# Kernel optimization log

Measured on AMD Instinct MI355X. Metric: run time of the kernel, lower is better.

## Reference

```python
import jax, jax.numpy as jnp
import numpy as np

EMBED_DIM = 1024
NUM_HEADS = 16
HEAD_DIM = EMBED_DIM // NUM_HEADS


def setup_inputs() -> dict:
    key = jax.random.key(0)
    ks = jax.random.split(key, 5)
    B, S, D = 2, 2048, EMBED_DIM
    scale = 1.0 / np.sqrt(D)
    x = jax.random.normal(ks[0], (B, S, D), dtype=jnp.float32)
    qkv_w = jax.random.uniform(ks[1], (3 * D, D), dtype=jnp.float32, minval=-scale, maxval=scale)
    qkv_b = jax.random.uniform(ks[2], (3 * D,), dtype=jnp.float32, minval=-scale, maxval=scale)
    out_w = jax.random.uniform(ks[3], (D, D), dtype=jnp.float32, minval=-scale, maxval=scale)
    out_b = jax.random.uniform(ks[4], (D,), dtype=jnp.float32, minval=-scale, maxval=scale)
    return {"x": x, "qkv_w": qkv_w, "qkv_b": qkv_b, "out_w": out_w, "out_b": out_b}


def reference(x, qkv_w, qkv_b, out_w, out_b):
    B, S, D = x.shape
    H, hd = NUM_HEADS, HEAD_DIM
    # QKV projection (torch Linear: y = x @ W^T + b)
    qkv = jnp.einsum('bsd,ed->bse', x, qkv_w) + qkv_b          # [B,S,3D]
    qkv = qkv.reshape(B, S, 3, H, hd)
    q, k, v = (jnp.moveaxis(qkv[:, :, i], 2, 1) for i in range(3))  # each [B,H,S,hd]
    scores = jnp.einsum('bhqd,bhkd->bhqk', q, k) / np.sqrt(hd)  # [B,H,S,S]
    probs = jax.nn.softmax(scores, axis=-1)
    attn = jnp.einsum('bhqk,bhkd->bhqd', probs, v)              # [B,H,S,hd]
    attn = jnp.moveaxis(attn, 1, 2).reshape(B, S, D)
    return jnp.einsum('bsd,ed->bse', attn, out_w) + out_b
```

## Files before the change

kernel.cpp:

```cpp
#include <hip/hip_runtime.h>
#include <stdint.h>

typedef __bf16 bf16;
typedef __attribute__((ext_vector_type(2))) __bf16 bf16x2;
typedef __attribute__((ext_vector_type(4))) __bf16 bf16x4;
typedef __attribute__((ext_vector_type(8))) __bf16 bf16x8;
typedef __attribute__((ext_vector_type(4))) float f32x4;
typedef __attribute__((ext_vector_type(16))) float f32x16;

#define LOG2E_OVER_8 0.18033688011112042f

#if __has_builtin(__builtin_amdgcn_exp2f)
#define EXP2(x) __builtin_amdgcn_exp2f(x)
#else
#define EXP2(x) exp2f(x)
#endif

__device__ __forceinline__ void gl_lds16(const bf16* g, bf16* l) {
  __builtin_amdgcn_global_load_lds(
      (const __attribute__((address_space(1))) void*)g,
      (__attribute__((address_space(3))) void*)l, 16, 0, 0);
}
#define WAIT_VM0_BARRIER() asm volatile("s_waitcnt vmcnt(0)\n\ts_barrier" ::: "memory")

__device__ __forceinline__ uint32_t pack2(float a, float b) {
  union { bf16x2 v; uint32_t u; } z;
  z.v[0] = (bf16)a; z.v[1] = (bf16)b;
  return z.u;
}

__global__ __launch_bounds__(256) void cvt_kernel(const float* __restrict__ s,
                                                  bf16* __restrict__ d, int n) {
  int i = (blockIdx.x * 256 + threadIdx.x) * 8;
  if (i >= n) return;
  float4 a = *(const float4*)(s + i);
  float4 b = *(const float4*)(s + i + 4);
  bf16x8 o;
  o[0] = (bf16)a.x; o[1] = (bf16)a.y; o[2] = (bf16)a.z; o[3] = (bf16)a.w;
  o[4] = (bf16)b.x; o[5] = (bf16)b.y; o[6] = (bf16)b.z; o[7] = (bf16)b.w;
  *(bf16x8*)(d + i) = o;
}

template <int EPI>
__global__ __launch_bounds__(256, 3) void gemm_bt(
    const bf16* __restrict__ A, const bf16* __restrict__ Bw,
    const float* __restrict__ bias,
    bf16* __restrict__ qo, bf16* __restrict__ ko, bf16* __restrict__ vTo,
    float* __restrict__ outF) {
  constexpr int MT = EPI ? 64 : 128;
  constexpr int MI = MT / 32;
  constexpr int ASZ = MT * 32;
  constexpr int BSZ = 128 * 32;
  constexpr int RS = 136;
  constexpr int SME = EPI ? (2 * ASZ + 2 * BSZ) : (128 * RS);
  __shared__ __attribute__((aligned(16))) bf16 smem[SME];

  int bx, by;
  {
    const int f = blockIdx.x;
    const int xcd = f & 7, idx = f >> 3;
    if constexpr (EPI == 0) { by = xcd * 4 + (idx & 3); bx = idx >> 2; }
    else                    { by = xcd * 8 + (idx & 7); bx = idx >> 3; }
  }

  const int t = threadIdx.x;
  const int L = t & 63;
  const int li = L & 15;
  const int qd = L >> 4;
  const int w = t >> 6;
  const int wm = (w >> 1) * (MT / 2);
  const int wn = (w & 1) * 64;
  const int bm0 = by * MT;
  const int bn0 = bx * 128;
  const int r_st = t >> 2;
  const int c_st = (t & 3) * 8;

  const bf16* Ab = A + (size_t)bm0 * 1024;
  const bf16* Bb = Bw + (size_t)bn0 * 1024;

  auto issue = [&](int k0, int bi) {
    bf16* As_ = smem + bi * ASZ;
    bf16* Bs_ = smem + 2 * ASZ + bi * BSZ;
    gl_lds16(Ab + (size_t)r_st * 1024 + k0 + c_st, As_ + t * 8);
    if constexpr (MT == 128)
      gl_lds16(Ab + (size_t)(r_st + 64) * 1024 + k0 + c_st, As_ + (t + 256) * 8);
    gl_lds16(Bb + (size_t)r_st * 1024 + k0 + c_st, Bs_ + t * 8);
    gl_lds16(Bb + (size_t)(r_st + 64) * 1024 + k0 + c_st, Bs_ + (t + 256) * 8);
  };

  f32x4 acc[MI][4] = {};
  issue(0, 0);
  for (int it = 0; it < 32; ++it) {
    WAIT_VM0_BARRIER();
    if (it < 31) issue((it + 1) * 32, (it + 1) & 1);
    const bf16* Ac = smem + (it & 1) * ASZ;
    const bf16* Bc = smem + 2 * ASZ + (it & 1) * BSZ;
    bf16x8 af[MI], bfr[4];
#pragma unroll
    for (int mi = 0; mi < MI; ++mi)
      af[mi] = *(const bf16x8*)(Ac + (wm + mi * 16 + li) * 32 + qd * 8);
#pragma unroll
    for (int ni = 0; ni < 4; ++ni)
      bfr[ni] = *(const bf16x8*)(Bc + (wn + ni * 16 + li) * 32 + qd * 8);
#pragma unroll
    for (int mi = 0; mi < MI; ++mi)
#pragma unroll
      for (int ni = 0; ni < 4; ++ni)
        acc[mi][ni] = __builtin_amdgcn_mfma_f32_16x16x32_bf16(af[mi], bfr[ni],
                                                              acc[mi][ni], 0, 0, 0);
  }

  if constexpr (EPI == 0) {
    const int which = bn0 >> 10;
    __syncthreads();
    bf16* Ct = smem;
    if (which == 2) {
#pragma unroll
      for (int mi = 0; mi < MI; ++mi) {
        const int m_l = wm + mi * 16 + qd * 4;
#pragma unroll
        for (int ni = 0; ni < 4; ++ni) {
          const int n_l = wn + ni * 16 + li;
          const float bi = bias[bn0 + n_l];
          bf16x4 pk;
#pragma unroll
          for (int r = 0; r < 4; ++r) pk[r] = (bf16)(acc[mi][ni][r] + bi);
          *(bf16x4*)(Ct + n_l * RS + m_l) = pk;
        }
      }
    } else {
      const float sc = (which == 0) ? LOG2E_OVER_8 : 1.0f;
#pragma unroll
      for (int mi = 0; mi < MI; ++mi) {
        const int m_l = wm + mi * 16 + qd * 4;
#pragma unroll
        for (int ni = 0; ni < 4; ++ni) {
          const int n_l = wn + ni * 16 + li;
          const float bi = bias[bn0 + n_l];
#pragma unroll
          for (int r = 0; r < 4; ++r)
            Ct[(m_l + r) * RS + n_l] = (bf16)((acc[mi][ni][r] + bi) * sc);
        }
      }
    }
    __syncthreads();
    const int jr = t >> 4;
    const int jc = t & 15;
#pragma unroll
    for (int pass = 0; pass < 8; ++pass) {
      const int row = pass * 16 + jr;
      bf16x8 vv = *(const bf16x8*)(Ct + row * RS + jc * 8);
      if (which == 2) {
        const int n_g = bn0 + row;
        const int hh = (n_g >> 6) & 15, dd = n_g & 63;
        const int bb = bm0 >> 11;
        const int s_b = (bm0 & 2047) + jc * 8;
        *(bf16x8*)(vTo + ((size_t)(bb * 16 + hh) * 64 + dd) * 2048 + s_b) = vv;
      } else {
        const int m_g = bm0 + row;
        const int bb = m_g >> 11, ss = m_g & 2047;
        const int n_g = bn0 + jc * 8;
        const int hh = (n_g >> 6) & 15, dd = n_g & 63;
        bf16* dst = (which == 0 ? qo : ko);
        *(bf16x8*)(dst + ((size_t)(bb * 16 + hh) * 2048 + ss) * 64 + dd) = vv;
      }
    }
  } else {
#pragma unroll
    for (int mi = 0; mi < MI; ++mi) {
      const int m_g = bm0 + wm + mi * 16 + qd * 4;
#pragma unroll
      for (int ni = 0; ni < 4; ++ni) {
        const int n_g = bn0 + wn + ni * 16 + li;
        const float bi = bias[n_g];
#pragma unroll
        for (int r = 0; r < 4; ++r)
          outF[(size_t)(m_g + r) * 1024 + n_g] = acc[mi][ni][r] + bi;
      }
    }
  }
}

__global__ __launch_bounds__(128, 2) void attn_fwd(
    const bf16* __restrict__ Q, const bf16* __restrict__ K,
    const bf16* __restrict__ VT, bf16* __restrict__ AO) {
  __shared__ __attribute__((aligned(16))) bf16 Ks[2 * 4096];
  __shared__ __attribute__((aligned(16))) bf16 Vs[2 * 4096];
  const int t = threadIdx.x;
  const int L = t & 63;
  const int m31 = L & 31;
  const int hi = L >> 5;
  const int w = t >> 6;

  const int lid = blockIdx.x;
  const int bh_ = ((lid & 7) << 2) + (lid >> 8);
  const int qb = (lid >> 3) & 31;
  const int b = bh_ >> 4, h = bh_ & 15;
  const size_t bh = (size_t)(b * 16 + h);

  const bf16* Qp = Q + bh * 2048 * 64;
  const bf16* Kp = K + bh * 2048 * 64;
  const bf16* Vp = VT + bh * 64 * 2048;
  const int q0 = qb * 64 + w * 32;

  bf16x8 qf[4];
#pragma unroll
  for (int s = 0; s < 4; ++s)
    qf[s] = *(const bf16x8*)(Qp + (size_t)(q0 + m31) * 64 + s * 16 + hi * 8);

  f32x16 acc[2] = {};
  float lsum = 0.f;

  const int srow = t >> 3;
  const int scc = (t & 7) ^ (srow & 7);
  auto issue = [&](int kt, int bi) {
    const bf16* Kt = Kp + (size_t)kt * 4096;
    const bf16* Vt = Vp + kt * 64;
    bf16* Kd = Ks + bi * 4096;
    bf16* Vd = Vs + bi * 4096;
#pragma unroll
    for (int r = 0; r < 4; ++r) {
      gl_lds16(Kt + (srow + 16 * r) * 64 + scc * 8, Kd + (t + 128 * r) * 8);
      gl_lds16(Vt + (size_t)(srow + 16 * r) * 2048 + scc * 8, Vd + (t + 128 * r) * 8);
    }
  };

  const int rlow = m31 & 7;
  issue(0, 0);
  for (int kt = 0; kt < 32; ++kt) {
    WAIT_VM0_BARRIER();
    if (kt < 31) issue(kt + 1, (kt + 1) & 1);
    const bf16* Kc = Ks + (kt & 1) * 4096;
    const bf16* Vc = Vs + (kt & 1) * 4096;

    f32x16 st[2];
#pragma unroll
    for (int kt2 = 0; kt2 < 2; ++kt2) {
      f32x16 z = {};
#pragma unroll
      for (int s = 0; s < 4; ++s) {
        bf16x8 kf = *(const bf16x8*)(
            Kc + ((kt2 * 32 + m31) * 8 + ((2 * s + hi) ^ rlow)) * 8);
        z = __builtin_amdgcn_mfma_f32_32x32x16_bf16(kf, qf[s], z, 0, 0, 0);
      }
      st[kt2] = z;
    }

    uint32_t pk[2][8];
#pragma unroll
    for (int kt2 = 0; kt2 < 2; ++kt2)
#pragma unroll
      for (int j = 0; j < 8; ++j) {
        float a = EXP2(st[kt2][2 * j]);
        float c = EXP2(st[kt2][2 * j + 1]);
        lsum += a + c;
        pk[kt2][j] = pack2(a, c);
      }

    uint32_t sw[2][8];
#pragma unroll
    for (int kt2 = 0; kt2 < 2; ++kt2)
#pragma unroll
      for (int j = 0; j < 8; ++j)
        sw[kt2][j] = (uint32_t)__shfl_xor((int)pk[kt2][j], 32);

    union FU { uint32_t u[4]; bf16x8 v; };
    FU af[2][2];
#pragma unroll
    for (int kt2 = 0; kt2 < 2; ++kt2) {
      if (hi == 0) {
        af[kt2][0].u[0] = pk[kt2][0]; af[kt2][0].u[1] = pk[kt2][1];
        af[kt2][0].u[2] = sw[kt2][0]; af[kt2][0].u[3] = sw[kt2][1];
        af[kt2][1].u[0] = pk[kt2][4]; af[kt2][1].u[1] = pk[kt2][5];
        af[kt2][1].u[2] = sw[kt2][4]; af[kt2][1].u[3] = sw[kt2][5];
      } else {
        af[kt2][0].u[0] = sw[kt2][2]; af[kt2][0].u[1] = sw[kt2][3];
        af[kt2][0].u[2] = pk[kt2][2]; af[kt2][0].u[3] = pk[kt2][3];
        af[kt2][1].u[0] = sw[kt2][6]; af[kt2][1].u[1] = sw[kt2][7];
        af[kt2][1].u[2] = pk[kt2][6]; af[kt2][1].u[3] = pk[kt2][7];
      }
    }

#pragma unroll
    for (int dt = 0; dt < 2; ++dt)
#pragma unroll
      for (int kt2 = 0; kt2 < 2; ++kt2)
#pragma unroll
        for (int u = 0; u < 2; ++u) {
          bf16x8 vf = *(const bf16x8*)(
              Vc + ((dt * 32 + m31) * 8 + ((kt2 * 4 + u * 2 + hi) ^ rlow)) * 8);
          acc[dt] = __builtin_amdgcn_mfma_f32_32x32x16_bf16(af[kt2][u].v, vf,
                                                            acc[dt], 0, 0, 0);
        }
  }

  lsum += __shfl_xor(lsum, 32);
  const float inv = 1.f / lsum;

#pragma unroll
  for (int r = 0; r < 16; ++r) {
    const int qrow = (r & 3) + 8 * (r >> 2) + 4 * hi;
    const float invq = __shfl(inv, qrow);
    const size_t base = ((size_t)b * 2048 + q0 + qrow) * 1024 + h * 64 + m31;
    AO[base] = (bf16)(acc[0][r] * invq);
    AO[base + 32] = (bf16)(acc[1][r] * invq);
  }
}

extern "C" void kernel_launch(void* const* d_in, const int* in_sizes, int n_in,
                              void* d_out, int out_size, void* d_ws, size_t ws_size,
                              hipStream_t stream) {
  const float* x = (const float*)d_in[0];
  const float* qkvw = (const float*)d_in[1];
  const float* qkvb = (const float*)d_in[2];
  const float* outw = (const float*)d_in[3];
  const float* outb = (const float*)d_in[4];
  float* out = (float*)d_out;

  bf16* xb = (bf16*)d_ws;
  bf16* wq = xb + (size_t)4096 * 1024;
  bf16* wo = wq + (size_t)3072 * 1024;
  bf16* q = wo + (size_t)1024 * 1024;
  bf16* kk = q + (size_t)2 * 16 * 2048 * 64;
  bf16* vT = kk + (size_t)2 * 16 * 2048 * 64;
  bf16* attn = xb;

  cvt_kernel<<<2048, 256, 0, stream>>>(x, xb, 4096 * 1024);
  cvt_kernel<<<1536, 256, 0, stream>>>(qkvw, wq, 3072 * 1024);
  cvt_kernel<<<512, 256, 0, stream>>>(outw, wo, 1024 * 1024);

  gemm_bt<0><<<768, 256, 0, stream>>>(xb, wq, qkvb, q, kk, vT, nullptr);
  attn_fwd<<<1024, 128, 0, stream>>>(q, kk, vT, attn);
  gemm_bt<1><<<512, 256, 0, stream>>>(attn, wo, outb, nullptr, nullptr, nullptr, out);
}
```

Baseline: 192.4 us.

## Merge conversion launches and feed PV MFMA directly without cross-lane shuffles

Replaces three fp32-to-bf16 conversion launches with a single kernel that picks its source buffer from the global index, saving launch overhead. In attention, the P·V product now uses the 32x32x8 bf16 MFMA, whose A-operand layout matches the score accumulator layout. Exponentiated scores can therefore be packed and consumed directly, with no __shfl_xor exchanges or lane-dependent fragment assembly. The tradeoff is twice as many smaller MFMA instructions and narrower 8-byte LDS reads of V.

```diff
diff --git a/kernel.cpp b/kernel.cpp
--- a/kernel.cpp
+++ b/kernel.cpp
@@ -7,6 +7,7 @@
 typedef __attribute__((ext_vector_type(8))) __bf16 bf16x8;
 typedef __attribute__((ext_vector_type(4))) float f32x4;
 typedef __attribute__((ext_vector_type(16))) float f32x16;
+typedef __attribute__((ext_vector_type(4))) short short4v;
 
 #define LOG2E_OVER_8 0.18033688011112042f
 
@@ -29,12 +30,20 @@
   return z.u;
 }
 
-__global__ __launch_bounds__(256) void cvt_kernel(const float* __restrict__ s,
-                                                  bf16* __restrict__ d, int n) {
+#define N_X  (4096 * 1024)
+#define N_WQ (3072 * 1024)
+#define N_WO (1024 * 1024)
+__global__ __launch_bounds__(256) void cvt3_kernel(const float* __restrict__ x,
+                                                   const float* __restrict__ wq,
+                                                   const float* __restrict__ wo,
+                                                   bf16* __restrict__ d) {
   int i = (blockIdx.x * 256 + threadIdx.x) * 8;
-  if (i >= n) return;
-  float4 a = *(const float4*)(s + i);
-  float4 b = *(const float4*)(s + i + 4);
+  const float* s;
+  if (i < N_X) s = x + i;
+  else if (i < N_X + N_WQ) s = wq + (i - N_X);
+  else s = wo + (i - N_X - N_WQ);
+  float4 a = *(const float4*)s;
+  float4 b = *(const float4*)(s + 4);
   bf16x8 o;
   o[0] = (bf16)a.x; o[1] = (bf16)a.y; o[2] = (bf16)a.z; o[3] = (bf16)a.w;
   o[4] = (bf16)b.x; o[5] = (bf16)b.y; o[6] = (bf16)b.z; o[7] = (bf16)b.w;
@@ -246,52 +255,27 @@
       st[kt2] = z;
     }
 
-    uint32_t pk[2][8];
 #pragma unroll
     for (int kt2 = 0; kt2 < 2; ++kt2)
 #pragma unroll
-      for (int j = 0; j < 8; ++j) {
-        float a = EXP2(st[kt2][2 * j]);
-        float c = EXP2(st[kt2][2 * j + 1]);
-        lsum += a + c;
-        pk[kt2][j] = pack2(a, c);
-      }
-
-    uint32_t sw[2][8];
-#pragma unroll
-    for (int kt2 = 0; kt2 < 2; ++kt2)
-#pragma unroll
-      for (int j = 0; j < 8; ++j)
-        sw[kt2][j] = (uint32_t)__shfl_xor((int)pk[kt2][j], 32);
-
-    union FU { uint32_t u[4]; bf16x8 v; };
-    FU af[2][2];
-#pragma unroll
-    for (int kt2 = 0; kt2 < 2; ++kt2) {
-      if (hi == 0) {
-        af[kt2][0].u[0] = pk[kt2][0]; af[kt2][0].u[1] = pk[kt2][1];
-        af[kt2][0].u[2] = sw[kt2][0]; af[kt2][0].u[3] = sw[kt2][1];
-        af[kt2][1].u[0] = pk[kt2][4]; af[kt2][1].u[1] = pk[kt2][5];
-        af[kt2][1].u[2] = sw[kt2][4]; af[kt2][1].u[3] = sw[kt2][5];
-      } else {
-        af[kt2][0].u[0] = sw[kt2][2]; af[kt2][0].u[1] = sw[kt2][3];
-        af[kt2][0].u[2] = pk[kt2][2]; af[kt2][0].u[3] = pk[kt2][3];
-        af[kt2][1].u[0] = sw[kt2][6]; af[kt2][1].u[1] = sw[kt2][7];
-        af[kt2][1].u[2] = pk[kt2][6]; af[kt2][1].u[3] = pk[kt2][7];
-      }
-    }
-
-#pragma unroll
-    for (int dt = 0; dt < 2; ++dt)
-#pragma unroll
-      for (int kt2 = 0; kt2 < 2; ++kt2)
-#pragma unroll
-        for (int u = 0; u < 2; ++u) {
-          bf16x8 vf = *(const bf16x8*)(
-              Vc + ((dt * 32 + m31) * 8 + ((kt2 * 4 + u * 2 + hi) ^ rlow)) * 8);
-          acc[dt] = __builtin_amdgcn_mfma_f32_32x32x16_bf16(af[kt2][u].v, vf,
-                                                            acc[dt], 0, 0, 0);
+      for (int u = 0; u < 4; ++u) {
+        float e0 = EXP2(st[kt2][4 * u]);
+        float e1 = EXP2(st[kt2][4 * u + 1]);
+        float e2 = EXP2(st[kt2][4 * u + 2]);
+        float e3 = EXP2(st[kt2][4 * u + 3]);
+        lsum += (e0 + e1) + (e2 + e3);
+        union { uint32_t uu[2]; short4v s4; } pk;
+        pk.uu[0] = pack2(e0, e1);
+        pk.uu[1] = pack2(e2, e3);
+        const int g = kt2 * 4 + u;
+#pragma unroll
+        for (int dt = 0; dt < 2; ++dt) {
+          short4v vf = *(const short4v*)(
+              Vc + ((dt * 32 + m31) * 8 + (g ^ rlow)) * 8 + hi * 4);
+          acc[dt] = __builtin_amdgcn_mfma_f32_32x32x8bf16_1k(pk.s4, vf,
+                                                             acc[dt], 0, 0, 0);
         }
+      }
   }
 
   lsum += __shfl_xor(lsum, 32);
@@ -318,16 +302,14 @@
   float* out = (float*)d_out;
 
   bf16* xb = (bf16*)d_ws;
-  bf16* wq = xb + (size_t)4096 * 1024;
-  bf16* wo = wq + (size_t)3072 * 1024;
-  bf16* q = wo + (size_t)1024 * 1024;
+  bf16* wq = xb + (size_t)N_X;
+  bf16* wo = wq + (size_t)N_WQ;
+  bf16* q = wo + (size_t)N_WO;
   bf16* kk = q + (size_t)2 * 16 * 2048 * 64;
   bf16* vT = kk + (size_t)2 * 16 * 2048 * 64;
   bf16* attn = xb;
 
-  cvt_kernel<<<2048, 256, 0, stream>>>(x, xb, 4096 * 1024);
-  cvt_kernel<<<1536, 256, 0, stream>>>(qkvw, wq, 3072 * 1024);
-  cvt_kernel<<<512, 256, 0, stream>>>(outw, wo, 1024 * 1024);
+  cvt3_kernel<<<4096, 256, 0, stream>>>(x, qkvw, outw, xb);
 
   gemm_bt<0><<<768, 256, 0, stream>>>(xb, wq, qkvb, q, kk, vT, nullptr);
   attn_fwd<<<1024, 128, 0, stream>>>(q, kk, vT, attn);
```

Result: no change. 194.2 us (+1.0%).

## Split-K the output projection with atomics and merge three conversion launches

Applied to the files above, without the earlier changes.

The three fp32-to-bf16 conversion launches become a single kernel that picks its source by index. The output projection GEMM is split along K into two halves, which doubles the grid to 1024 blocks. The halves accumulate into the output with float atomicAdd after a memset, and only the first split adds the bias. This aims for more parallelism and fewer launches, at the cost of an extra memset, atomic traffic and a summation order that is no longer deterministic.

```diff
diff --git a/kernel.cpp b/kernel.cpp
--- a/kernel.cpp
+++ b/kernel.cpp
@@ -29,12 +29,20 @@
   return z.u;
 }
 
-__global__ __launch_bounds__(256) void cvt_kernel(const float* __restrict__ s,
-                                                  bf16* __restrict__ d, int n) {
+#define N_X  (4096 * 1024)
+#define N_WQ (3072 * 1024)
+#define N_WO (1024 * 1024)
+__global__ __launch_bounds__(256) void cvt3_kernel(const float* __restrict__ x,
+                                                   const float* __restrict__ wq,
+                                                   const float* __restrict__ wo,
+                                                   bf16* __restrict__ d) {
   int i = (blockIdx.x * 256 + threadIdx.x) * 8;
-  if (i >= n) return;
-  float4 a = *(const float4*)(s + i);
-  float4 b = *(const float4*)(s + i + 4);
+  const float* s;
+  if (i < N_X) s = x + i;
+  else if (i < N_X + N_WQ) s = wq + (i - N_X);
+  else s = wo + (i - N_X - N_WQ);
+  float4 a = *(const float4*)s;
+  float4 b = *(const float4*)(s + 4);
   bf16x8 o;
   o[0] = (bf16)a.x; o[1] = (bf16)a.y; o[2] = (bf16)a.z; o[3] = (bf16)a.w;
   o[4] = (bf16)b.x; o[5] = (bf16)b.y; o[6] = (bf16)b.z; o[7] = (bf16)b.w;
@@ -53,14 +61,15 @@
   constexpr int BSZ = 128 * 32;
   constexpr int RS = 136;
   constexpr int SME = EPI ? (2 * ASZ + 2 * BSZ) : (128 * RS);
+  constexpr int NIT = EPI ? 16 : 32;
   __shared__ __attribute__((aligned(16))) bf16 smem[SME];
 
-  int bx, by;
+  int bx, by, ks = 0;
   {
     const int f = blockIdx.x;
     const int xcd = f & 7, idx = f >> 3;
     if constexpr (EPI == 0) { by = xcd * 4 + (idx & 3); bx = idx >> 2; }
-    else                    { by = xcd * 8 + (idx & 7); bx = idx >> 3; }
+    else { by = xcd * 8 + (idx & 7); bx = (idx >> 3) & 7; ks = idx >> 6; }
   }
 
   const int t = threadIdx.x;
@@ -72,6 +81,7 @@
   const int wn = (w & 1) * 64;
   const int bm0 = by * MT;
   const int bn0 = bx * 128;
+  const int kbase = ks * 512;
   const int r_st = t >> 2;
   const int c_st = (t & 3) * 8;
 
@@ -89,10 +99,10 @@
   };
 
   f32x4 acc[MI][4] = {};
-  issue(0, 0);
-  for (int it = 0; it < 32; ++it) {
+  issue(kbase, 0);
+  for (int it = 0; it < NIT; ++it) {
     WAIT_VM0_BARRIER();
-    if (it < 31) issue((it + 1) * 32, (it + 1) & 1);
+    if (it < NIT - 1) issue(kbase + (it + 1) * 32, (it + 1) & 1);
     const bf16* Ac = smem + (it & 1) * ASZ;
     const bf16* Bc = smem + 2 * ASZ + (it & 1) * BSZ;
     bf16x8 af[MI], bfr[4];
@@ -166,16 +176,17 @@
       }
     }
   } else {
+    const float bsc = (ks == 0) ? 1.0f : 0.0f;
 #pragma unroll
     for (int mi = 0; mi < MI; ++mi) {
       const int m_g = bm0 + wm + mi * 16 + qd * 4;
 #pragma unroll
       for (int ni = 0; ni < 4; ++ni) {
         const int n_g = bn0 + wn + ni * 16 + li;
-        const float bi = bias[n_g];
+        const float bi = bias[n_g] * bsc;
 #pragma unroll
         for (int r = 0; r < 4; ++r)
-          outF[(size_t)(m_g + r) * 1024 + n_g] = acc[mi][ni][r] + bi;
+          atomicAdd(&outF[(size_t)(m_g + r) * 1024 + n_g], acc[mi][ni][r] + bi);
       }
     }
   }
@@ -318,18 +329,18 @@
   float* out = (float*)d_out;
 
   bf16* xb = (bf16*)d_ws;
-  bf16* wq = xb + (size_t)4096 * 1024;
-  bf16* wo = wq + (size_t)3072 * 1024;
-  bf16* q = wo + (size_t)1024 * 1024;
+  bf16* wq = xb + (size_t)N_X;
+  bf16* wo = wq + (size_t)N_WQ;
+  bf16* q = wo + (size_t)N_WO;
   bf16* kk = q + (size_t)2 * 16 * 2048 * 64;
   bf16* vT = kk + (size_t)2 * 16 * 2048 * 64;
   bf16* attn = xb;
 
-  cvt_kernel<<<2048, 256, 0, stream>>>(x, xb, 4096 * 1024);
-  cvt_kernel<<<1536, 256, 0, stream>>>(qkvw, wq, 3072 * 1024);
-  cvt_kernel<<<512, 256, 0, stream>>>(outw, wo, 1024 * 1024);
+  hipMemsetAsync(out, 0, (size_t)out_size * sizeof(float), stream);
+
+  cvt3_kernel<<<4096, 256, 0, stream>>>(x, qkvw, outw, xb);
 
   gemm_bt<0><<<768, 256, 0, stream>>>(xb, wq, qkvb, q, kk, vT, nullptr);
   attn_fwd<<<1024, 128, 0, stream>>>(q, kk, vT, attn);
-  gemm_bt<1><<<512, 256, 0, stream>>>(attn, wo, outb, nullptr, nullptr, nullptr, out);
-}
+  gemm_bt<1><<<1024, 256, 0, stream>>>(attn, wo, outb, nullptr, nullptr, nullptr, out);
+}
```

After: 216.0 us. 12.3% more time.
